# Optimization experiments

Hardware: AMD Instinct MI355X
Metric: run time of the kernel (lower is better)

The kernel has to match this reference:

```python
import jax, jax.numpy as jnp
import numpy as np

B, Tq, Tk, D, H = 8, 128, 512, 256, 256

def setup_inputs() -> dict:
    key = jax.random.key(0)
    k1, k2, k3, k4, k5, k6, k7 = jax.random.split(key, 7)
    scale = 1.0 / np.sqrt(D)
    return {
        "queries": jax.random.normal(k1, (B, Tq, D), dtype=jnp.float32),
        "keys": jax.random.normal(k2, (B, Tk, D), dtype=jnp.float32),
        "values": jax.random.normal(k3, (B, Tk, D), dtype=jnp.float32),
        "valid_lens": jax.random.randint(k4, (B,), 1, Tk + 1),
        "Wq": jax.random.normal(k5, (D, H), dtype=jnp.float32) * scale,
        "Wk": jax.random.normal(k6, (D, H), dtype=jnp.float32) * scale,
        "wv": jax.random.normal(k7, (H,), dtype=jnp.float32) * (1.0 / np.sqrt(H)),
    }

def masked_softmax(scores, valid_lens):
    # scores: (B, Tq, Tk); valid_lens: (B,)
    T = scores.shape[-1]
    mask = jnp.arange(T) < valid_lens[:, None, None]  # (B,1,Tk) -> broadcast
    neg_inf = jnp.finfo(scores.dtype).min
    probs = jax.nn.softmax(jnp.where(mask, scores, neg_inf), axis=-1)
    fully_masked = ~jnp.any(mask, axis=-1, keepdims=True)
    return jnp.where(fully_masked, jnp.zeros_like(probs), probs)

def reference(queries, keys, values, valid_lens, Wq, Wk, wv):
    q_proj = jnp.einsum('bqd,dh->bqh', queries, Wq)  # (B,Tq,H)
    k_proj = jnp.einsum('bkd,dh->bkh', keys, Wk)      # (B,Tk,H)
    features = jnp.tanh(q_proj[:, :, None, :] + k_proj[:, None, :, :])  # (B,Tq,Tk,H)
    scores = jnp.einsum('bqkh,h->bqk', features, wv)  # (B,Tq,Tk)
    attn = masked_softmax(scores, valid_lens)
    # dropout is identity at p=0.0 / eval
    return jnp.einsum('bqk,bkd->bqd', attn, values)
```

## Files before the change

### kernel.cpp

```cpp
#include <hip/hip_runtime.h>
#include <hip/hip_bf16.h>

#define B_  8
#define TQ_ 128
#define TK_ 512
#define D_  256
#define H_  256

#define KSCALE 2.8853900817779268f

__device__ __forceinline__ float fast_exp2(float x) {
    return __builtin_amdgcn_exp2f(x);
}

__device__ __forceinline__ float fast_rcp(float y) {
    float r = __int_as_float(0x7EF311C3 - __float_as_int(y));
    r = r * fmaf(-y, r, 2.0f);
    r = r * fmaf(-y, r, 2.0f);
    return r;
}

__device__ __forceinline__ float wave_red_min(float v) {
#pragma unroll
    for (int o = 32; o > 0; o >>= 1) v = fminf(v, __shfl_xor(v, o));
    return v;
}
__device__ __forceinline__ float wave_red_sum(float v) {
#pragma unroll
    for (int o = 32; o > 0; o >>= 1) v += __shfl_xor(v, o);
    return v;
}

__global__ __launch_bounds__(512) void proj_kernel(
    const float* __restrict__ queries, const float* __restrict__ keys,
    const float* __restrict__ Wq, const float* __restrict__ Wk,
    float* __restrict__ qp, float* __restrict__ kpT)
{
    __shared__ __align__(16) float4 xs4[16 * 64];
    __shared__ __align__(16) float tile[16 * 260];

    const int t = threadIdx.x;
    const bool isQ = (blockIdx.x < 64);
    const float* X; const float* W; int b, r0;
    if (isQ) {
        b = blockIdx.x >> 3; r0 = (blockIdx.x & 7) * 16;
        X = queries + ((size_t)b * TQ_ + r0) * D_;  W = Wq;
    } else {
        int id = blockIdx.x - 64;
        b = id >> 5; r0 = (id & 31) * 16;
        X = keys + ((size_t)b * TK_ + r0) * D_;     W = Wk;
    }

    const float4* X4 = reinterpret_cast<const float4*>(X);
    xs4[t]       = X4[t];
    xs4[t + 512] = X4[t + 512];
    __syncthreads();

    const int hq = t & 63;
    const int rg = t >> 6;
    const int rA = rg * 2, rB = rA + 1;
    const float4* W4 = reinterpret_cast<const float4*>(W) + hq;

    float4 a0 = make_float4(0.f, 0.f, 0.f, 0.f);
    float4 a1 = make_float4(0.f, 0.f, 0.f, 0.f);

#pragma unroll 4
    for (int d4 = 0; d4 < 64; ++d4) {
        const float4 xa = xs4[rA * 64 + d4];
        const float4 xb = xs4[rB * 64 + d4];
        const float4 w0 = W4[(size_t)(d4 * 4 + 0) * 64];
        const float4 w1 = W4[(size_t)(d4 * 4 + 1) * 64];
        const float4 w2 = W4[(size_t)(d4 * 4 + 2) * 64];
        const float4 w3 = W4[(size_t)(d4 * 4 + 3) * 64];
        a0.x = fmaf(w0.x, xa.x, a0.x); a0.y = fmaf(w0.y, xa.x, a0.y);
        a0.z = fmaf(w0.z, xa.x, a0.z); a0.w = fmaf(w0.w, xa.x, a0.w);
        a1.x = fmaf(w0.x, xb.x, a1.x); a1.y = fmaf(w0.y, xb.x, a1.y);
        a1.z = fmaf(w0.z, xb.x, a1.z); a1.w = fmaf(w0.w, xb.x, a1.w);
        a0.x = fmaf(w1.x, xa.y, a0.x); a0.y = fmaf(w1.y, xa.y, a0.y);
        a0.z = fmaf(w1.z, xa.y, a0.z); a0.w = fmaf(w1.w, xa.y, a0.w);
        a1.x = fmaf(w1.x, xb.y, a1.x); a1.y = fmaf(w1.y, xb.y, a1.y);
        a1.z = fmaf(w1.z, xb.y, a1.z); a1.w = fmaf(w1.w, xb.y, a1.w);
        a0.x = fmaf(w2.x, xa.z, a0.x); a0.y = fmaf(w2.y, xa.z, a0.y);
        a0.z = fmaf(w2.z, xa.z, a0.z); a0.w = fmaf(w2.w, xa.z, a0.w);
        a1.x = fmaf(w2.x, xb.z, a1.x); a1.y = fmaf(w2.y, xb.z, a1.y);
        a1.z = fmaf(w2.z, xb.z, a1.z); a1.w = fmaf(w2.w, xb.z, a1.w);
        a0.x = fmaf(w3.x, xa.w, a0.x); a0.y = fmaf(w3.y, xa.w, a0.y);
        a0.z = fmaf(w3.z, xa.w, a0.z); a0.w = fmaf(w3.w, xa.w, a0.w);
        a1.x = fmaf(w3.x, xb.w, a1.x); a1.y = fmaf(w3.y, xb.w, a1.y);
        a1.z = fmaf(w3.z, xb.w, a1.z); a1.w = fmaf(w3.w, xb.w, a1.w);
    }
    a0.x *= KSCALE; a0.y *= KSCALE; a0.z *= KSCALE; a0.w *= KSCALE;
    a1.x *= KSCALE; a1.y *= KSCALE; a1.z *= KSCALE; a1.w *= KSCALE;

    if (isQ) {
        float* dst = qp + ((size_t)b * TQ_ + r0) * H_ + hq * 4;
        *reinterpret_cast<float4*>(dst + (size_t)rA * H_) = a0;
        *reinterpret_cast<float4*>(dst + (size_t)rB * H_) = a1;
    } else {
        *reinterpret_cast<float4*>(&tile[rA * 260 + hq * 4]) = a0;
        *reinterpret_cast<float4*>(&tile[rB * 260 + hq * 4]) = a1;
        __syncthreads();
        const int h = t >> 1, half = t & 1;
        float v[8];
#pragma unroll
        for (int i = 0; i < 8; ++i) v[i] = tile[(half * 8 + i) * 260 + h];
        float* dst = kpT + (size_t)b * (H_ * TK_) + (size_t)h * TK_ + r0 + half * 8;
        *reinterpret_cast<float4*>(dst)     = make_float4(v[0], v[1], v[2], v[3]);
        *reinterpret_cast<float4*>(dst + 4) = make_float4(v[4], v[5], v[6], v[7]);
    }
}

__global__ __launch_bounds__(512) void attn_kernel(
    const float* __restrict__ qp, const float* __restrict__ kpT,
    const float* __restrict__ values, const int* __restrict__ valid_lens,
    const float* __restrict__ wv, float* __restrict__ out)
{
    __shared__ __align__(16) float2 qw[H_];
    __shared__ __align__(16) float wvs[H_];
    __shared__ __align__(16) float2 pe2[TK_];
    __shared__ float redm[2][8], reds[2][8];
    __shared__ float acch[2 * 256];

    const int t = threadIdx.x;
    const int b = blockIdx.y;
    const int q0 = blockIdx.x * 2;

    const int len = valid_lens[b];

    const float* qpb = qp + ((size_t)b * TQ_ + q0) * H_;
    if (t < 256) qw[t] = make_float2(qpb[t], qpb[256 + t]);
    else         wvs[t - 256] = wv[t - 256];
    __syncthreads();

    const int k = t;
    const float* kcol = kpT + (size_t)b * (H_ * TK_) + k;
    float a0 = 0.f, a1 = 0.f;
#pragma unroll 8
    for (int h = 0; h < H_; ++h) {
        const float kk = kcol[(size_t)h * TK_];
        const float2 q2 = qw[h];
        const float w = wvs[h];
        const float e0 = fast_exp2(q2.x + kk);
        const float e1 = fast_exp2(q2.y + kk);
        a0 = fmaf(w, fast_rcp(1.0f + e0), a0);
        a1 = fmaf(w, fast_rcp(1.0f + e1), a1);
    }

    const int lane = t & 63, wid = t >> 6;
    const bool valid = (k < len);
    const float BIG = 3.0e38f;

    float m0 = wave_red_min(valid ? a0 : BIG);
    float m1 = wave_red_min(valid ? a1 : BIG);
    if (lane == 0) { redm[0][wid] = m0; redm[1][wid] = m1; }
    __syncthreads();
    float mr0 = redm[0][0], mr1 = redm[1][0];
#pragma unroll
    for (int i = 1; i < 8; ++i) { mr0 = fminf(mr0, redm[0][i]); mr1 = fminf(mr1, redm[1][i]); }

    const float e0 = valid ? fast_exp2((mr0 - a0) * KSCALE) : 0.f;
    const float e1 = valid ? fast_exp2((mr1 - a1) * KSCALE) : 0.f;
    pe2[k] = make_float2(e0, e1);
    float S0 = wave_red_sum(e0);
    float S1 = wave_red_sum(e1);
    if (lane == 0) { reds[0][wid] = S0; reds[1][wid] = S1; }
    __syncthreads();
    float s0 = 0.f, s1 = 0.f;
#pragma unroll
    for (int i = 0; i < 8; ++i) { s0 += reds[0][i]; s1 += reds[1][i]; }
    const float rs0 = 1.0f / s0, rs1 = 1.0f / s1;

    const int d = t & 255;
    const int half = t >> 8;
    float c0 = 0.f, c1 = 0.f;
    const float* vb = values + (size_t)b * (TK_ * D_) + (size_t)(half * 256) * D_ + d;
    const float2* pb = &pe2[half * 256];
#pragma unroll 8
    for (int kk = 0; kk < 256; ++kk) {
        const float v = vb[(size_t)kk * D_];
        const float2 p = pb[kk];
        c0 = fmaf(p.x, v, c0);
        c1 = fmaf(p.y, v, c1);
    }
    if (half == 1) { acch[d] = c0; acch[256 + d] = c1; }
    __syncthreads();
    if (half == 0) {
        float* ob = out + ((size_t)b * TQ_ + q0) * D_ + d;
        ob[0]  = (c0 + acch[d])       * rs0;
        ob[D_] = (c1 + acch[256 + d]) * rs1;
    }
}

extern "C" void kernel_launch(void* const* d_in, const int* in_sizes, int n_in,
                              void* d_out, int out_size, void* d_ws, size_t ws_size,
                              hipStream_t stream) {
    const float* queries    = (const float*)d_in[0];
    const float* keys       = (const float*)d_in[1];
    const float* values     = (const float*)d_in[2];
    const int*   valid_lens = (const int*)  d_in[3];
    const float* Wq         = (const float*)d_in[4];
    const float* Wk         = (const float*)d_in[5];
    const float* wv         = (const float*)d_in[6];
    float* out = (float*)d_out;

    float* qp  = (float*)d_ws;
    float* kpT = qp + (size_t)B_ * TQ_ * H_;

    proj_kernel<<<320, 512, 0, stream>>>(queries, keys, Wq, Wk, qp, kpT);
    attn_kernel<<<dim3(TQ_ / 2, B_), 512, 0, stream>>>(qp, kpT, values, valid_lens, wv, out);
}
```

Measured before the change: 145.9 us.

## Skip masked keys, store key projection row-major, use hardware rcp

Key projection blocks whose rows all fall past valid_len now exit early, and the key projection is stored row-major rather than transposed, which removes the LDS transpose. In the attention kernel, a wave skips the tanh-score loop when all 64 of its keys are masked, and the PV accumulation skips 64-key chunks past valid_len. Each thread now reads its key row with float4 loads. The Newton-iteration reciprocal is replaced by the hardware rcp instruction, which may slightly change accuracy.

```diff
diff --git a/kernel.cpp b/kernel.cpp
--- a/kernel.cpp
+++ b/kernel.cpp
@@ -12,12 +12,8 @@
 __device__ __forceinline__ float fast_exp2(float x) {
     return __builtin_amdgcn_exp2f(x);
 }
-
 __device__ __forceinline__ float fast_rcp(float y) {
-    float r = __int_as_float(0x7EF311C3 - __float_as_int(y));
-    r = r * fmaf(-y, r, 2.0f);
-    r = r * fmaf(-y, r, 2.0f);
-    return r;
+    return __builtin_amdgcn_rcpf(y);
 }
 
 __device__ __forceinline__ float wave_red_min(float v) {
@@ -34,21 +30,24 @@
 __global__ __launch_bounds__(512) void proj_kernel(
     const float* __restrict__ queries, const float* __restrict__ keys,
     const float* __restrict__ Wq, const float* __restrict__ Wk,
-    float* __restrict__ qp, float* __restrict__ kpT)
+    const int* __restrict__ valid_lens,
+    float* __restrict__ qp, float* __restrict__ kp)
 {
     __shared__ __align__(16) float4 xs4[16 * 64];
-    __shared__ __align__(16) float tile[16 * 260];
 
     const int t = threadIdx.x;
     const bool isQ = (blockIdx.x < 64);
-    const float* X; const float* W; int b, r0;
+    const float* X; const float* W; float* dst; int b, r0;
     if (isQ) {
         b = blockIdx.x >> 3; r0 = (blockIdx.x & 7) * 16;
         X = queries + ((size_t)b * TQ_ + r0) * D_;  W = Wq;
+        dst = qp + ((size_t)b * TQ_ + r0) * H_;
     } else {
         int id = blockIdx.x - 64;
         b = id >> 5; r0 = (id & 31) * 16;
+        if (r0 >= valid_lens[b]) return;
         X = keys + ((size_t)b * TK_ + r0) * D_;     W = Wk;
+        dst = kp + ((size_t)b * TK_ + r0) * H_;
     }
 
     const float4* X4 = reinterpret_cast<const float4*>(X);
@@ -92,61 +91,54 @@
     a0.x *= KSCALE; a0.y *= KSCALE; a0.z *= KSCALE; a0.w *= KSCALE;
     a1.x *= KSCALE; a1.y *= KSCALE; a1.z *= KSCALE; a1.w *= KSCALE;
 
-    if (isQ) {
-        float* dst = qp + ((size_t)b * TQ_ + r0) * H_ + hq * 4;
-        *reinterpret_cast<float4*>(dst + (size_t)rA * H_) = a0;
-        *reinterpret_cast<float4*>(dst + (size_t)rB * H_) = a1;
-    } else {
-        *reinterpret_cast<float4*>(&tile[rA * 260 + hq * 4]) = a0;
-        *reinterpret_cast<float4*>(&tile[rB * 260 + hq * 4]) = a1;
-        __syncthreads();
-        const int h = t >> 1, half = t & 1;
-        float v[8];
-#pragma unroll
-        for (int i = 0; i < 8; ++i) v[i] = tile[(half * 8 + i) * 260 + h];
-        float* dst = kpT + (size_t)b * (H_ * TK_) + (size_t)h * TK_ + r0 + half * 8;
-        *reinterpret_cast<float4*>(dst)     = make_float4(v[0], v[1], v[2], v[3]);
-        *reinterpret_cast<float4*>(dst + 4) = make_float4(v[4], v[5], v[6], v[7]);
-    }
+    *reinterpret_cast<float4*>(dst + (size_t)rA * H_ + hq * 4) = a0;
+    *reinterpret_cast<float4*>(dst + (size_t)rB * H_ + hq * 4) = a1;
 }
 
 __global__ __launch_bounds__(512) void attn_kernel(
-    const float* __restrict__ qp, const float* __restrict__ kpT,
+    const float* __restrict__ qp, const float* __restrict__ kp,
     const float* __restrict__ values, const int* __restrict__ valid_lens,
     const float* __restrict__ wv, float* __restrict__ out)
 {
-    __shared__ __align__(16) float2 qw[H_];
-    __shared__ __align__(16) float wvs[H_];
+    __shared__ __align__(16) float qw0[H_], qw1[H_], wvs[H_];
     __shared__ __align__(16) float2 pe2[TK_];
     __shared__ float redm[2][8], reds[2][8];
-    __shared__ float acch[2 * 256];
+    __shared__ float acch[2][256];
 
     const int t = threadIdx.x;
     const int b = blockIdx.y;
     const int q0 = blockIdx.x * 2;
-
     const int len = valid_lens[b];
 
     const float* qpb = qp + ((size_t)b * TQ_ + q0) * H_;
-    if (t < 256) qw[t] = make_float2(qpb[t], qpb[256 + t]);
+    if (t < 256) { qw0[t] = qpb[t]; qw1[t] = qpb[H_ + t]; }
     else         wvs[t - 256] = wv[t - 256];
     __syncthreads();
 
-    const int k = t;
-    const float* kcol = kpT + (size_t)b * (H_ * TK_) + k;
+    const int k = t, lane = t & 63, wid = t >> 6;
     float a0 = 0.f, a1 = 0.f;
-#pragma unroll 8
-    for (int h = 0; h < H_; ++h) {
-        const float kk = kcol[(size_t)h * TK_];
-        const float2 q2 = qw[h];
-        const float w = wvs[h];
-        const float e0 = fast_exp2(q2.x + kk);
-        const float e1 = fast_exp2(q2.y + kk);
-        a0 = fmaf(w, fast_rcp(1.0f + e0), a0);
-        a1 = fmaf(w, fast_rcp(1.0f + e1), a1);
-    }
-
-    const int lane = t & 63, wid = t >> 6;
+    if (wid * 64 < len) {
+        const float4* kr  = reinterpret_cast<const float4*>(kp + ((size_t)b * TK_ + k) * H_);
+        const float4* q04 = reinterpret_cast<const float4*>(qw0);
+        const float4* q14 = reinterpret_cast<const float4*>(qw1);
+        const float4* wv4 = reinterpret_cast<const float4*>(wvs);
+#pragma unroll 4
+        for (int h4 = 0; h4 < 64; ++h4) {
+            const float4 kk = kr[h4];
+            const float4 qa = q04[h4];
+            const float4 qb = q14[h4];
+            const float4 w  = wv4[h4];
+            a0 = fmaf(w.x, fast_rcp(1.0f + fast_exp2(qa.x + kk.x)), a0);
+            a1 = fmaf(w.x, fast_rcp(1.0f + fast_exp2(qb.x + kk.x)), a1);
+            a0 = fmaf(w.y, fast_rcp(1.0f + fast_exp2(qa.y + kk.y)), a0);
+            a1 = fmaf(w.y, fast_rcp(1.0f + fast_exp2(qb.y + kk.y)), a1);
+            a0 = fmaf(w.z, fast_rcp(1.0f + fast_exp2(qa.z + kk.z)), a0);
+            a1 = fmaf(w.z, fast_rcp(1.0f + fast_exp2(qb.z + kk.z)), a1);
+            a0 = fmaf(w.w, fast_rcp(1.0f + fast_exp2(qa.w + kk.w)), a0);
+            a1 = fmaf(w.w, fast_rcp(1.0f + fast_exp2(qb.w + kk.w)), a1);
+        }
+    }
+
     const bool valid = (k < len);
     const float BIG = 3.0e38f;
 
@@ -175,19 +167,25 @@
     float c0 = 0.f, c1 = 0.f;
     const float* vb = values + (size_t)b * (TK_ * D_) + (size_t)(half * 256) * D_ + d;
     const float2* pb = &pe2[half * 256];
+#pragma unroll
+    for (int c = 0; c < 4; ++c) {
+        if (half * 256 + c * 64 < len) {
 #pragma unroll 8
-    for (int kk = 0; kk < 256; ++kk) {
-        const float v = vb[(size_t)kk * D_];
-        const float2 p = pb[kk];
-        c0 = fmaf(p.x, v, c0);
-        c1 = fmaf(p.y, v, c1);
-    }
-    if (half == 1) { acch[d] = c0; acch[256 + d] = c1; }
+            for (int i = 0; i < 64; ++i) {
+                const int kk = c * 64 + i;
+                const float v = vb[(size_t)kk * D_];
+                const float2 p = pb[kk];
+                c0 = fmaf(p.x, v, c0);
+                c1 = fmaf(p.y, v, c1);
+            }
+        }
+    }
+    if (half == 1) { acch[0][d] = c0; acch[1][d] = c1; }
     __syncthreads();
     if (half == 0) {
         float* ob = out + ((size_t)b * TQ_ + q0) * D_ + d;
-        ob[0]  = (c0 + acch[d])       * rs0;
-        ob[D_] = (c1 + acch[256 + d]) * rs1;
+        ob[0]  = (c0 + acch[0][d]) * rs0;
+        ob[D_] = (c1 + acch[1][d]) * rs1;
     }
 }
 
@@ -203,9 +201,9 @@
     const float* wv         = (const float*)d_in[6];
     float* out = (float*)d_out;
 
-    float* qp  = (float*)d_ws;
-    float* kpT = qp + (size_t)B_ * TQ_ * H_;
-
-    proj_kernel<<<320, 512, 0, stream>>>(queries, keys, Wq, Wk, qp, kpT);
-    attn_kernel<<<dim3(TQ_ / 2, B_), 512, 0, stream>>>(qp, kpT, values, valid_lens, wv, out);
-}
+    float* qp = (float*)d_ws;
+    float* kp = qp + (size_t)B_ * TQ_ * H_;
+
+    proj_kernel<<<320, 512, 0, stream>>>(queries, keys, Wq, Wk, valid_lens, qp, kp);
+    attn_kernel<<<dim3(TQ_ / 2, B_), 512, 0, stream>>>(qp, kp, values, valid_lens, wv, out);
+}
```

After: 139.9 us. -4.2%, faster.

## Skip masked keys in projection and scoring, use hardware rcp, restructure score loop

Applied to the files above, without the earlier changes.

The key-projection kernel now exits early for row blocks that lie beyond the batch's valid length. The score kernel gives each thread four keys over a quarter of the hidden dimension using float4 loads and combines the partials in shared memory. Waves whose key half is fully masked skip the tanh loop, and the values reduction skips 64-key chunks past the valid length. The Newton-iteration reciprocal is replaced by the hardware rcp instruction, which trades precision for fewer ALU ops, and shared memory use grows.

```diff
diff --git a/kernel.cpp b/kernel.cpp
--- a/kernel.cpp
+++ b/kernel.cpp
@@ -12,12 +12,8 @@
 __device__ __forceinline__ float fast_exp2(float x) {
     return __builtin_amdgcn_exp2f(x);
 }
-
 __device__ __forceinline__ float fast_rcp(float y) {
-    float r = __int_as_float(0x7EF311C3 - __float_as_int(y));
-    r = r * fmaf(-y, r, 2.0f);
-    r = r * fmaf(-y, r, 2.0f);
-    return r;
+    return __builtin_amdgcn_rcpf(y);
 }
 
 __device__ __forceinline__ float wave_red_min(float v) {
@@ -34,6 +30,7 @@
 __global__ __launch_bounds__(512) void proj_kernel(
     const float* __restrict__ queries, const float* __restrict__ keys,
     const float* __restrict__ Wq, const float* __restrict__ Wk,
+    const int* __restrict__ valid_lens,
     float* __restrict__ qp, float* __restrict__ kpT)
 {
     __shared__ __align__(16) float4 xs4[16 * 64];
@@ -48,6 +45,7 @@
     } else {
         int id = blockIdx.x - 64;
         b = id >> 5; r0 = (id & 31) * 16;
+        if (r0 >= valid_lens[b]) return;
         X = keys + ((size_t)b * TK_ + r0) * D_;     W = Wk;
     }
 
@@ -115,38 +113,56 @@
     const float* __restrict__ values, const int* __restrict__ valid_lens,
     const float* __restrict__ wv, float* __restrict__ out)
 {
-    __shared__ __align__(16) float2 qw[H_];
+    __shared__ __align__(16) float2 qw2[H_];
     __shared__ __align__(16) float wvs[H_];
+    __shared__ __align__(16) float paccA[4 * TK_];
+    __shared__ __align__(16) float paccB[4 * TK_];
     __shared__ __align__(16) float2 pe2[TK_];
     __shared__ float redm[2][8], reds[2][8];
-    __shared__ float acch[2 * 256];
+    __shared__ float acch[2][256];
 
     const int t = threadIdx.x;
     const int b = blockIdx.y;
     const int q0 = blockIdx.x * 2;
-
     const int len = valid_lens[b];
 
     const float* qpb = qp + ((size_t)b * TQ_ + q0) * H_;
-    if (t < 256) qw[t] = make_float2(qpb[t], qpb[256 + t]);
+    if (t < 256) qw2[t] = make_float2(qpb[t], qpb[H_ + t]);
     else         wvs[t - 256] = wv[t - 256];
     __syncthreads();
 
+    const int kq = t & 127;
+    const int hg = t >> 7;
+    const int wid = t >> 6, lane = t & 63;
+    float4 A0 = make_float4(0.f, 0.f, 0.f, 0.f);
+    float4 A1 = make_float4(0.f, 0.f, 0.f, 0.f);
+
+    if ((wid & 1) * 256 < len) {
+        const float* kbase = kpT + (size_t)b * (H_ * TK_) + (size_t)(hg * 64) * TK_ + kq * 4;
+#pragma unroll 4
+        for (int i = 0; i < 64; ++i) {
+            const float4 kk = *reinterpret_cast<const float4*>(kbase + (size_t)i * TK_);
+            const int h = hg * 64 + i;
+            const float2 q2 = qw2[h];
+            const float w = wvs[h];
+            A0.x = fmaf(w, fast_rcp(1.0f + fast_exp2(q2.x + kk.x)), A0.x);
+            A0.y = fmaf(w, fast_rcp(1.0f + fast_exp2(q2.x + kk.y)), A0.y);
+            A0.z = fmaf(w, fast_rcp(1.0f + fast_exp2(q2.x + kk.z)), A0.z);
+            A0.w = fmaf(w, fast_rcp(1.0f + fast_exp2(q2.x + kk.w)), A0.w);
+            A1.x = fmaf(w, fast_rcp(1.0f + fast_exp2(q2.y + kk.x)), A1.x);
+            A1.y = fmaf(w, fast_rcp(1.0f + fast_exp2(q2.y + kk.y)), A1.y);
+            A1.z = fmaf(w, fast_rcp(1.0f + fast_exp2(q2.y + kk.z)), A1.z);
+            A1.w = fmaf(w, fast_rcp(1.0f + fast_exp2(q2.y + kk.w)), A1.w);
+        }
+    }
+    *reinterpret_cast<float4*>(&paccA[hg * TK_ + kq * 4]) = A0;
+    *reinterpret_cast<float4*>(&paccB[hg * TK_ + kq * 4]) = A1;
+    __syncthreads();
+
     const int k = t;
-    const float* kcol = kpT + (size_t)b * (H_ * TK_) + k;
-    float a0 = 0.f, a1 = 0.f;
-#pragma unroll 8
-    for (int h = 0; h < H_; ++h) {
-        const float kk = kcol[(size_t)h * TK_];
-        const float2 q2 = qw[h];
-        const float w = wvs[h];
-        const float e0 = fast_exp2(q2.x + kk);
-        const float e1 = fast_exp2(q2.y + kk);
-        a0 = fmaf(w, fast_rcp(1.0f + e0), a0);
-        a1 = fmaf(w, fast_rcp(1.0f + e1), a1);
-    }
-
-    const int lane = t & 63, wid = t >> 6;
+    float a0 = ((paccA[k] + paccA[TK_ + k]) + (paccA[2 * TK_ + k] + paccA[3 * TK_ + k]));
+    float a1 = ((paccB[k] + paccB[TK_ + k]) + (paccB[2 * TK_ + k] + paccB[3 * TK_ + k]));
+
     const bool valid = (k < len);
     const float BIG = 3.0e38f;
 
@@ -175,19 +191,25 @@
     float c0 = 0.f, c1 = 0.f;
     const float* vb = values + (size_t)b * (TK_ * D_) + (size_t)(half * 256) * D_ + d;
     const float2* pb = &pe2[half * 256];
+#pragma unroll
+    for (int c = 0; c < 4; ++c) {
+        if (half * 256 + c * 64 < len) {
 #pragma unroll 8
-    for (int kk = 0; kk < 256; ++kk) {
-        const float v = vb[(size_t)kk * D_];
-        const float2 p = pb[kk];
-        c0 = fmaf(p.x, v, c0);
-        c1 = fmaf(p.y, v, c1);
-    }
-    if (half == 1) { acch[d] = c0; acch[256 + d] = c1; }
+            for (int i = 0; i < 64; ++i) {
+                const int kk = c * 64 + i;
+                const float v = vb[(size_t)kk * D_];
+                const float2 p = pb[kk];
+                c0 = fmaf(p.x, v, c0);
+                c1 = fmaf(p.y, v, c1);
+            }
+        }
+    }
+    if (half == 1) { acch[0][d] = c0; acch[1][d] = c1; }
     __syncthreads();
     if (half == 0) {
         float* ob = out + ((size_t)b * TQ_ + q0) * D_ + d;
-        ob[0]  = (c0 + acch[d])       * rs0;
-        ob[D_] = (c1 + acch[256 + d]) * rs1;
+        ob[0]  = (c0 + acch[0][d]) * rs0;
+        ob[D_] = (c1 + acch[1][d]) * rs1;
     }
 }
 
@@ -206,6 +228,6 @@
     float* qp  = (float*)d_ws;
     float* kpT = qp + (size_t)B_ * TQ_ * H_;
 
-    proj_kernel<<<320, 512, 0, stream>>>(queries, keys, Wq, Wk, qp, kpT);
+    proj_kernel<<<320, 512, 0, stream>>>(queries, keys, Wq, Wk, valid_lens, qp, kpT);
     attn_kernel<<<dim3(TQ_ / 2, B_), 512, 0, stream>>>(qp, kpT, values, valid_lens, wv, out);
 }
```

Measured after the change: 139.4 us. 4.5% less time.

## Skip masked key rows and restructure attention to one query per block

Applied to the files above, without the earlier changes.

Skips projection of key tiles that lie beyond valid_lens and skips score and PV work for masked key chunks in the attention kernel. The attention kernel now handles one query per 256-thread block, with each thread computing two adjacent keys through float2 loads and one output column. The hand-rolled Newton reciprocal is replaced with the hardware rcp builtin. This trades the query-pair reuse of key and value loads for less wasted work on masked positions; the gain depends on how short the valid lengths are.

```diff
diff --git a/kernel.cpp b/kernel.cpp
--- a/kernel.cpp
+++ b/kernel.cpp
@@ -12,12 +12,8 @@
 __device__ __forceinline__ float fast_exp2(float x) {
     return __builtin_amdgcn_exp2f(x);
 }
-
 __device__ __forceinline__ float fast_rcp(float y) {
-    float r = __int_as_float(0x7EF311C3 - __float_as_int(y));
-    r = r * fmaf(-y, r, 2.0f);
-    r = r * fmaf(-y, r, 2.0f);
-    return r;
+    return __builtin_amdgcn_rcpf(y);
 }
 
 __device__ __forceinline__ float wave_red_min(float v) {
@@ -34,6 +30,7 @@
 __global__ __launch_bounds__(512) void proj_kernel(
     const float* __restrict__ queries, const float* __restrict__ keys,
     const float* __restrict__ Wq, const float* __restrict__ Wk,
+    const int* __restrict__ valid_lens,
     float* __restrict__ qp, float* __restrict__ kpT)
 {
     __shared__ __align__(16) float4 xs4[16 * 64];
@@ -48,6 +45,7 @@
     } else {
         int id = blockIdx.x - 64;
         b = id >> 5; r0 = (id & 31) * 16;
+        if (r0 >= valid_lens[b]) return;
         X = keys + ((size_t)b * TK_ + r0) * D_;     W = Wk;
     }
 
@@ -110,85 +108,71 @@
     }
 }
 
-__global__ __launch_bounds__(512) void attn_kernel(
+__global__ __launch_bounds__(256) void attn_kernel(
     const float* __restrict__ qp, const float* __restrict__ kpT,
     const float* __restrict__ values, const int* __restrict__ valid_lens,
     const float* __restrict__ wv, float* __restrict__ out)
 {
-    __shared__ __align__(16) float2 qw[H_];
-    __shared__ __align__(16) float wvs[H_];
-    __shared__ __align__(16) float2 pe2[TK_];
-    __shared__ float redm[2][8], reds[2][8];
-    __shared__ float acch[2 * 256];
+    __shared__ __align__(16) float qw[H_], wvs[H_];
+    __shared__ __align__(16) float2 pe2[TK_ / 2];
+    __shared__ float redm[4], reds[4];
 
     const int t = threadIdx.x;
-    const int b = blockIdx.y;
-    const int q0 = blockIdx.x * 2;
-
+    const int b = blockIdx.x;
+    const int q = blockIdx.y;
     const int len = valid_lens[b];
 
-    const float* qpb = qp + ((size_t)b * TQ_ + q0) * H_;
-    if (t < 256) qw[t] = make_float2(qpb[t], qpb[256 + t]);
-    else         wvs[t - 256] = wv[t - 256];
+    const float* qpb = qp + ((size_t)b * TQ_ + q) * H_;
+    qw[t]  = qpb[t];
+    wvs[t] = wv[t];
     __syncthreads();
 
-    const int k = t;
-    const float* kcol = kpT + (size_t)b * (H_ * TK_) + k;
+    const int wid = t >> 6, lane = t & 63;
+    const int k0 = 2 * t;
     float a0 = 0.f, a1 = 0.f;
-#pragma unroll 8
-    for (int h = 0; h < H_; ++h) {
-        const float kk = kcol[(size_t)h * TK_];
-        const float2 q2 = qw[h];
-        const float w = wvs[h];
-        const float e0 = fast_exp2(q2.x + kk);
-        const float e1 = fast_exp2(q2.y + kk);
-        a0 = fmaf(w, fast_rcp(1.0f + e0), a0);
-        a1 = fmaf(w, fast_rcp(1.0f + e1), a1);
+    if (wid * 128 < len) {
+        const float* kb = kpT + (size_t)b * (H_ * TK_) + k0;
+#pragma unroll 4
+        for (int h = 0; h < H_; ++h) {
+            const float2 kk = *reinterpret_cast<const float2*>(kb + (size_t)h * TK_);
+            const float qv = qw[h];
+            const float w  = wvs[h];
+            a0 = fmaf(w, fast_rcp(1.0f + fast_exp2(qv + kk.x)), a0);
+            a1 = fmaf(w, fast_rcp(1.0f + fast_exp2(qv + kk.y)), a1);
+        }
     }
 
-    const int lane = t & 63, wid = t >> 6;
-    const bool valid = (k < len);
+    const bool v0 = (k0 < len), v1 = (k0 + 1 < len);
     const float BIG = 3.0e38f;
 
-    float m0 = wave_red_min(valid ? a0 : BIG);
-    float m1 = wave_red_min(valid ? a1 : BIG);
-    if (lane == 0) { redm[0][wid] = m0; redm[1][wid] = m1; }
+    float m = fminf(v0 ? a0 : BIG, v1 ? a1 : BIG);
+    m = wave_red_min(m);
+    if (lane == 0) redm[wid] = m;
     __syncthreads();
-    float mr0 = redm[0][0], mr1 = redm[1][0];
+    const float mr = fminf(fminf(redm[0], redm[1]), fminf(redm[2], redm[3]));
+
+    const float e0 = v0 ? fast_exp2((mr - a0) * KSCALE) : 0.f;
+    const float e1 = v1 ? fast_exp2((mr - a1) * KSCALE) : 0.f;
+    pe2[t] = make_float2(e0, e1);
+    float S = wave_red_sum(e0 + e1);
+    if (lane == 0) reds[wid] = S;
+    __syncthreads();
+    const float rs = 1.0f / (((reds[0] + reds[1]) + (reds[2] + reds[3])));
+
+    const float* pes = reinterpret_cast<const float*>(pe2);
+    const float* vb  = values + (size_t)b * (TK_ * D_) + t;
+    float c = 0.f;
 #pragma unroll
-    for (int i = 1; i < 8; ++i) { mr0 = fminf(mr0, redm[0][i]); mr1 = fminf(mr1, redm[1][i]); }
-
-    const float e0 = valid ? fast_exp2((mr0 - a0) * KSCALE) : 0.f;
-    const float e1 = valid ? fast_exp2((mr1 - a1) * KSCALE) : 0.f;
-    pe2[k] = make_float2(e0, e1);
-    float S0 = wave_red_sum(e0);
-    float S1 = wave_red_sum(e1);
-    if (lane == 0) { reds[0][wid] = S0; reds[1][wid] = S1; }
-    __syncthreads();
-    float s0 = 0.f, s1 = 0.f;
-#pragma unroll
-    for (int i = 0; i < 8; ++i) { s0 += reds[0][i]; s1 += reds[1][i]; }
-    const float rs0 = 1.0f / s0, rs1 = 1.0f / s1;
-
-    const int d = t & 255;
-    const int half = t >> 8;
-    float c0 = 0.f, c1 = 0.f;
-    const float* vb = values + (size_t)b * (TK_ * D_) + (size_t)(half * 256) * D_ + d;
-    const float2* pb = &pe2[half * 256];
+    for (int ch = 0; ch < 8; ++ch) {
+        if (ch * 64 < len) {
 #pragma unroll 8
-    for (int kk = 0; kk < 256; ++kk) {
-        const float v = vb[(size_t)kk * D_];
-        const float2 p = pb[kk];
-        c0 = fmaf(p.x, v, c0);
-        c1 = fmaf(p.y, v, c1);
+            for (int i = 0; i < 64; ++i) {
+                const int kk = ch * 64 + i;
+                c = fmaf(pes[kk], vb[(size_t)kk * D_], c);
+            }
+        }
     }
-    if (half == 1) { acch[d] = c0; acch[256 + d] = c1; }
-    __syncthreads();
-    if (half == 0) {
-        float* ob = out + ((size_t)b * TQ_ + q0) * D_ + d;
-        ob[0]  = (c0 + acch[d])       * rs0;
-        ob[D_] = (c1 + acch[256 + d]) * rs1;
-    }
+    out[((size_t)b * TQ_ + q) * D_ + t] = c * rs;
 }
 
 extern "C" void kernel_launch(void* const* d_in, const int* in_sizes, int n_in,
@@ -206,6 +190,6 @@
     float* qp  = (float*)d_ws;
     float* kpT = qp + (size_t)B_ * TQ_ * H_;
 
-    proj_kernel<<<320, 512, 0, stream>>>(queries, keys, Wq, Wk, qp, kpT);
-    attn_kernel<<<dim3(TQ_ / 2, B_), 512, 0, stream>>>(qp, kpT, values, valid_lens, wv, out);
+    proj_kernel<<<320, 512, 0, stream>>>(queries, keys, Wq, Wk, valid_lens, qp, kpT);
+    attn_kernel<<<dim3(B_, TQ_), 256, 0, stream>>>(qp, kpT, values, valid_lens, wv, out);
 }
```

Result: slower. 151.9 us (+4.1%).
